# Kernel tuning notes

Hardware: AMD Instinct MI355X
Metric: run time of the kernel (lower is better)

## Reference

```python
import jax, jax.numpy as jnp
import numpy as np


def setup_inputs() -> dict:
    key = jax.random.key(0)
    k1, k2 = jax.random.split(key)
    B, N, M, D = 4, 8192, 8192, 3
    input1 = jax.random.normal(k1, (B, N, D), dtype=jnp.float32)
    input2 = jax.random.normal(k2, (B, M, D), dtype=jnp.float32)
    return {"input1": input1, "input2": input2}


def reference(input1, input2):
    x2 = jnp.sum(input1 * input1, axis=-1)              # [B, N]
    y2 = jnp.sum(input2 * input2, axis=-1)              # [B, M]
    xy = jnp.einsum('bnd,bmd->bnm', input1, input2)     # [B, N, M]
    d2 = x2[:, :, None] + y2[:, None, :] - 2.0 * xy     # [B, N, M]
    d2 = jnp.maximum(d2, 0.0)
    dist1 = jnp.min(d2, axis=2)  # [B, N] nearest in input2 for each point in input1
    dist2 = jnp.min(d2, axis=1)  # [B, M] nearest in input1 for each point in input2
    # Chamfer loss: mean of both directional terms
    return jnp.mean(dist1) + jnp.mean(dist2)
```

## Files before the change

kernel.cpp:

```cpp
#include <hip/hip_runtime.h>

#define NB     4
#define NPTS   8192
#define NTP    (NPTS / 2)
#define TPB    256
#define QPC    16
#define ITERS  (NTP / TPB)

typedef float v4f __attribute__((ext_vector_type(4)));

__global__ void pack_pts(const float* __restrict__ in1, const float* __restrict__ in2,
                         v4f* __restrict__ nq, v4f* __restrict__ tp) {
    int i = blockIdx.x * blockDim.x + threadIdx.x;
    if (i < NB * NPTS) {
        float x = in1[3*i], y = in1[3*i+1], z = in1[3*i+2];
        nq[i] = (v4f){x, y, z, 0.5f * (x*x + y*y + z*z)};
    } else {
        int p = i - NB * NPTS;
        float x0 = in2[6*p+0], y0 = in2[6*p+1], z0 = in2[6*p+2];
        float x1 = in2[6*p+3], y1 = in2[6*p+4], z1 = in2[6*p+5];
        tp[2*p]   = (v4f){x0, x1, y0, y1};
        tp[2*p+1] = (v4f){z0, z1, 0.5f*(x0*x0 + y0*y0 + z0*z0),
                                  0.5f*(x1*x1 + y1*y1 + z1*z1)};
    }
}

template<int SLOTS>
__launch_bounds__(TPB, 4)
__global__ void chamfer_min(const v4f* __restrict__ nq, const v4f* __restrict__ tp,
                            unsigned* __restrict__ colbuf, float* __restrict__ accum) {
    constexpr int NCHUNK = (NPTS / SLOTS) / QPC;
    __shared__ unsigned colkey[NPTS];
    __shared__ float red[4][QPC];

    const int slot = blockIdx.x;
    const int bb   = blockIdx.y;
    const int t    = threadIdx.x;
    const int lane = t & 63;
    const int wave = t >> 6;

    uint4 ff = make_uint4(~0u, ~0u, ~0u, ~0u);
#pragma unroll
    for (int k = 0; k < NPTS / 4 / TPB; ++k) ((uint4*)colkey)[t + k * TPB] = ff;
    __syncthreads();

    const v4f* __restrict__ Tb = tp + (size_t)bb * (2 * NTP);
    const v4f* __restrict__ Qb = nq + (size_t)bb * NPTS + slot * (NCHUNK * QPC);

#pragma unroll 1
    for (int chunk = 0; chunk < NCHUNK; ++chunk) {
        float qx[QPC], qy[QPC], qz[QPC], qw[QPC];
#pragma unroll
        for (int j = 0; j < QPC; ++j) {
            v4f q = Qb[chunk * QPC + j];
            qx[j] = q.x; qy[j] = q.y; qz[j] = q.z; qw[j] = q.w;
            asm("" : "+v"(qx[j]), "+v"(qy[j]), "+v"(qz[j]), "+v"(qw[j]));
        }

        float accR[QPC];
#pragma unroll
        for (int j = 0; j < QPC; ++j) accR[j] = 1e30f;

        int idx = t;
        v4f tl = Tb[2 * idx], th = Tb[2 * idx + 1];

#pragma unroll 1
        for (int it = 0; it < ITERS; ++it) {
            int nidx = (idx + TPB) & (NTP - 1);
            v4f ntl = Tb[2 * nidx], nth = Tb[2 * nidx + 1];

            float x0 = tl.x, x1 = tl.y, y0 = tl.z, y1 = tl.w;
            float z0 = th.x, z1 = th.y, w0 = th.z, w1 = th.w;
            float c0 = 1e30f, c1 = 1e30f;
#pragma unroll
            for (int j = 0; j < QPC; j += 2) {
                float f0 = fmaf(-qx[j],   x0, fmaf(-qy[j],   y0, fmaf(-qz[j],   z0, w0 + qw[j])));
                float f1 = fmaf(-qx[j],   x1, fmaf(-qy[j],   y1, fmaf(-qz[j],   z1, w1 + qw[j])));
                float g0 = fmaf(-qx[j+1], x0, fmaf(-qy[j+1], y0, fmaf(-qz[j+1], z0, w0 + qw[j+1])));
                float g1 = fmaf(-qx[j+1], x1, fmaf(-qy[j+1], y1, fmaf(-qz[j+1], z1, w1 + qw[j+1])));
                asm("v_min3_f32 %0, %0, %1, %2" : "+v"(accR[j])   : "v"(f0), "v"(f1));
                asm("v_min3_f32 %0, %0, %1, %2" : "+v"(accR[j+1]) : "v"(g0), "v"(g1));
                asm("v_min3_f32 %0, %0, %1, %2" : "+v"(c0)        : "v"(f0), "v"(g0));
                asm("v_min3_f32 %0, %0, %1, %2" : "+v"(c1)        : "v"(f1), "v"(g1));
            }
            atomicMin(&colkey[idx],       __float_as_uint(fmaxf(c0, 0.0f)));
            atomicMin(&colkey[NTP + idx], __float_as_uint(fmaxf(c1, 0.0f)));
            tl = ntl; th = nth; idx = nidx;
        }

#pragma unroll
        for (int j = 0; j < QPC; ++j) {
            float a = accR[j];
            a = fminf(a, __shfl_xor(a, 32));
            a = fminf(a, __shfl_xor(a, 16));
            a = fminf(a, __shfl_xor(a, 8));
            a = fminf(a, __shfl_xor(a, 4));
            a = fminf(a, __shfl_xor(a, 2));
            a = fminf(a, __shfl_xor(a, 1));
            accR[j] = a;
        }
        if (lane == 0) {
#pragma unroll
            for (int j = 0; j < QPC; j += 4)
                *(v4f*)&red[wave][j] = (v4f){accR[j], accR[j+1], accR[j+2], accR[j+3]};
        }
        __syncthreads();
        if (t < QPC) {
            float m = fminf(fminf(red[0][t], red[1][t]), fminf(red[2][t], red[3][t]));
            float dist = fmaxf(2.0f * m, 0.0f);
#pragma unroll
            for (int off = 8; off > 0; off >>= 1)
                dist += __shfl_xor(dist, off, 16);
            if (t == 0) atomicAdd(accum, dist);
        }
        __syncthreads();
    }

    uint4* cb = (uint4*)(colbuf + (size_t)(bb * SLOTS + slot) * NPTS);
#pragma unroll
    for (int k = 0; k < NPTS / 4 / TPB; ++k) cb[t + k * TPB] = ((uint4*)colkey)[t + k * TPB];
}

template<int SLOTS>
__global__ void col_combine(const unsigned* __restrict__ colbuf, float* __restrict__ accum) {
    int tid = blockIdx.x * blockDim.x + threadIdx.x;
    int bb  = tid >> 13;
    int m   = tid & (NPTS - 1);
    const unsigned* cb = colbuf + (size_t)bb * SLOTS * NPTS + m;
    unsigned k = ~0u;
#pragma unroll 8
    for (int s = 0; s < SLOTS; ++s) k = min(k, cb[(size_t)s * NPTS]);
    float dist = 2.0f * __uint_as_float(k);
    for (int off = 32; off > 0; off >>= 1) dist += __shfl_xor(dist, off, 64);
    if ((threadIdx.x & 63) == 0) atomicAdd(accum, dist);
}

__global__ void finish(const float* __restrict__ accum, float* __restrict__ out) {
    out[0] = accum[0] * (1.0f / (NB * NPTS));
}

extern "C" void kernel_launch(void* const* d_in, const int* in_sizes, int n_in,
                              void* d_out, int out_size, void* d_ws, size_t ws_size,
                              hipStream_t stream) {
    const float* in1 = (const float*)d_in[0];
    const float* in2 = (const float*)d_in[1];

    char* ws = (char*)d_ws;
    float*    accum  = (float*)ws;
    v4f*      nq     = (v4f*)(ws + 256);
    v4f*      tp     = nq + (size_t)NB * NPTS;
    unsigned* colbuf = (unsigned*)(tp + (size_t)NB * NTP * 2);

    hipMemsetAsync(accum, 0, sizeof(float), stream);
    pack_pts<<<dim3((NB * NPTS + NB * NTP) / 256), 256, 0, stream>>>(in1, in2, nq, tp);

    const size_t base = 256 + (size_t)NB * NPTS * 16 * 2;
    const size_t need128 = base + (size_t)128 * NB * NPTS * 4;

    if (ws_size >= need128) {
        chamfer_min<128><<<dim3(128, NB), TPB, 0, stream>>>(nq, tp, colbuf, accum);
        col_combine<128><<<dim3(128), 256, 0, stream>>>(colbuf, accum);
    } else {
        chamfer_min<64><<<dim3(64, NB), TPB, 0, stream>>>(nq, tp, colbuf, accum);
        col_combine<64><<<dim3(128), 256, 0, stream>>>(colbuf, accum);
    }

    finish<<<1, 1, 0, stream>>>(accum, (float*)d_out);
}
```

Baseline: 74.42 us.

## Keep target points in registers and drop shared-memory column atomics

Each block now uses 1024 threads, and each thread holds a fixed set of target point pairs (KI=4) in registers for the whole kernel. Column minima build up in registers across chunks instead of through LDS atomicMin into a shared array. The grid is fixed at 64 slots per batch, and the accumulator reset moves into pack_pts to save a memset launch. The intent is to remove LDS atomics and repeated target reloads, at the cost of higher register pressure under __launch_bounds__(1024,4), fewer blocks (256 total), and a 16-wave reduction per chunk.

After: 80.48 us. +8.1%, slower.

```diff
diff --git a/kernel.cpp b/kernel.cpp
--- a/kernel.cpp
+++ b/kernel.cpp
@@ -3,15 +3,19 @@
 #define NB     4
 #define NPTS   8192
 #define NTP    (NPTS / 2)
-#define TPB    256
+#define TPB    1024
 #define QPC    16
-#define ITERS  (NTP / TPB)
+#define SLOTS  64
+#define NCHUNK (NPTS / SLOTS / QPC)
+#define KI     (NTP / TPB)
 
 typedef float v4f __attribute__((ext_vector_type(4)));
 
 __global__ void pack_pts(const float* __restrict__ in1, const float* __restrict__ in2,
-                         v4f* __restrict__ nq, v4f* __restrict__ tp) {
+                         v4f* __restrict__ nq, v4f* __restrict__ tp,
+                         float* __restrict__ accum) {
     int i = blockIdx.x * blockDim.x + threadIdx.x;
+    if (i == 0) accum[0] = 0.0f;
     if (i < NB * NPTS) {
         float x = in1[3*i], y = in1[3*i+1], z = in1[3*i+2];
         nq[i] = (v4f){x, y, z, 0.5f * (x*x + y*y + z*z)};
@@ -25,13 +29,10 @@
     }
 }
 
-template<int SLOTS>
 __launch_bounds__(TPB, 4)
 __global__ void chamfer_min(const v4f* __restrict__ nq, const v4f* __restrict__ tp,
                             unsigned* __restrict__ colbuf, float* __restrict__ accum) {
-    constexpr int NCHUNK = (NPTS / SLOTS) / QPC;
-    __shared__ unsigned colkey[NPTS];
-    __shared__ float red[4][QPC];
+    __shared__ float red[16][QPC];
 
     const int slot = blockIdx.x;
     const int bb   = blockIdx.y;
@@ -39,13 +40,19 @@
     const int lane = t & 63;
     const int wave = t >> 6;
 
-    uint4 ff = make_uint4(~0u, ~0u, ~0u, ~0u);
-#pragma unroll
-    for (int k = 0; k < NPTS / 4 / TPB; ++k) ((uint4*)colkey)[t + k * TPB] = ff;
-    __syncthreads();
-
     const v4f* __restrict__ Tb = tp + (size_t)bb * (2 * NTP);
     const v4f* __restrict__ Qb = nq + (size_t)bb * NPTS + slot * (NCHUNK * QPC);
+
+    v4f Tl[KI], Th[KI];
+#pragma unroll
+    for (int k = 0; k < KI; ++k) {
+        Tl[k] = Tb[2 * (t + k * TPB)];
+        Th[k] = Tb[2 * (t + k * TPB) + 1];
+    }
+
+    float c[2 * KI];
+#pragma unroll
+    for (int k = 0; k < 2 * KI; ++k) c[k] = 1e30f;
 
 #pragma unroll 1
     for (int chunk = 0; chunk < NCHUNK; ++chunk) {
@@ -54,24 +61,16 @@
         for (int j = 0; j < QPC; ++j) {
             v4f q = Qb[chunk * QPC + j];
             qx[j] = q.x; qy[j] = q.y; qz[j] = q.z; qw[j] = q.w;
-            asm("" : "+v"(qx[j]), "+v"(qy[j]), "+v"(qz[j]), "+v"(qw[j]));
         }
 
         float accR[QPC];
 #pragma unroll
         for (int j = 0; j < QPC; ++j) accR[j] = 1e30f;
 
-        int idx = t;
-        v4f tl = Tb[2 * idx], th = Tb[2 * idx + 1];
-
-#pragma unroll 1
-        for (int it = 0; it < ITERS; ++it) {
-            int nidx = (idx + TPB) & (NTP - 1);
-            v4f ntl = Tb[2 * nidx], nth = Tb[2 * nidx + 1];
-
-            float x0 = tl.x, x1 = tl.y, y0 = tl.z, y1 = tl.w;
-            float z0 = th.x, z1 = th.y, w0 = th.z, w1 = th.w;
-            float c0 = 1e30f, c1 = 1e30f;
+#pragma unroll
+        for (int k = 0; k < KI; ++k) {
+            float x0 = Tl[k].x, x1 = Tl[k].y, y0 = Tl[k].z, y1 = Tl[k].w;
+            float z0 = Th[k].x, z1 = Th[k].y, w0 = Th[k].z, w1 = Th[k].w;
 #pragma unroll
             for (int j = 0; j < QPC; j += 2) {
                 float f0 = fmaf(-qx[j],   x0, fmaf(-qy[j],   y0, fmaf(-qz[j],   z0, w0 + qw[j])));
@@ -80,12 +79,9 @@
                 float g1 = fmaf(-qx[j+1], x1, fmaf(-qy[j+1], y1, fmaf(-qz[j+1], z1, w1 + qw[j+1])));
                 asm("v_min3_f32 %0, %0, %1, %2" : "+v"(accR[j])   : "v"(f0), "v"(f1));
                 asm("v_min3_f32 %0, %0, %1, %2" : "+v"(accR[j+1]) : "v"(g0), "v"(g1));
-                asm("v_min3_f32 %0, %0, %1, %2" : "+v"(c0)        : "v"(f0), "v"(g0));
-                asm("v_min3_f32 %0, %0, %1, %2" : "+v"(c1)        : "v"(f1), "v"(g1));
+                asm("v_min3_f32 %0, %0, %1, %2" : "+v"(c[2*k])    : "v"(f0), "v"(g0));
+                asm("v_min3_f32 %0, %0, %1, %2" : "+v"(c[2*k+1])  : "v"(f1), "v"(g1));
             }
-            atomicMin(&colkey[idx],       __float_as_uint(fmaxf(c0, 0.0f)));
-            atomicMin(&colkey[NTP + idx], __float_as_uint(fmaxf(c1, 0.0f)));
-            tl = ntl; th = nth; idx = nidx;
         }
 
 #pragma unroll
@@ -106,7 +102,9 @@
         }
         __syncthreads();
         if (t < QPC) {
-            float m = fminf(fminf(red[0][t], red[1][t]), fminf(red[2][t], red[3][t]));
+            float m = red[0][t];
+#pragma unroll
+            for (int w = 1; w < 16; ++w) m = fminf(m, red[w][t]);
             float dist = fmaxf(2.0f * m, 0.0f);
 #pragma unroll
             for (int off = 8; off > 0; off >>= 1)
@@ -116,12 +114,16 @@
         __syncthreads();
     }
 
-    uint4* cb = (uint4*)(colbuf + (size_t)(bb * SLOTS + slot) * NPTS);
+    uint2* cb = (uint2*)(colbuf + (size_t)(bb * SLOTS + slot) * NPTS);
 #pragma unroll
-    for (int k = 0; k < NPTS / 4 / TPB; ++k) cb[t + k * TPB] = ((uint4*)colkey)[t + k * TPB];
+    for (int k = 0; k < KI; ++k) {
+        uint2 v;
+        v.x = __float_as_uint(fmaxf(c[2*k],   0.0f));
+        v.y = __float_as_uint(fmaxf(c[2*k+1], 0.0f));
+        cb[t + k * TPB] = v;
+    }
 }
 
-template<int SLOTS>
 __global__ void col_combine(const unsigned* __restrict__ colbuf, float* __restrict__ accum) {
     int tid = blockIdx.x * blockDim.x + threadIdx.x;
     int bb  = tid >> 13;
@@ -151,19 +153,11 @@
     v4f*      tp     = nq + (size_t)NB * NPTS;
     unsigned* colbuf = (unsigned*)(tp + (size_t)NB * NTP * 2);
 
-    hipMemsetAsync(accum, 0, sizeof(float), stream);
-    pack_pts<<<dim3((NB * NPTS + NB * NTP) / 256), 256, 0, stream>>>(in1, in2, nq, tp);
+    pack_pts<<<dim3((NB * NPTS + NB * NTP) / 256), 256, 0, stream>>>(in1, in2, nq, tp, accum);
 
-    const size_t base = 256 + (size_t)NB * NPTS * 16 * 2;
-    const size_t need128 = base + (size_t)128 * NB * NPTS * 4;
+    chamfer_min<<<dim3(SLOTS, NB), TPB, 0, stream>>>(nq, tp, colbuf, accum);
 
-    if (ws_size >= need128) {
-        chamfer_min<128><<<dim3(128, NB), TPB, 0, stream>>>(nq, tp, colbuf, accum);
-        col_combine<128><<<dim3(128), 256, 0, stream>>>(colbuf, accum);
-    } else {
-        chamfer_min<64><<<dim3(64, NB), TPB, 0, stream>>>(nq, tp, colbuf, accum);
-        col_combine<64><<<dim3(128), 256, 0, stream>>>(colbuf, accum);
-    }
+    col_combine<<<dim3(128), 256, 0, stream>>>(colbuf, accum);
 
     finish<<<1, 1, 0, stream>>>(accum, (float*)d_out);
 }
```
